# Performance work log

Hardware: AMD Instinct MI355X
Metric: run time of the kernel (lower is better)

## Reference

```python
import jax, jax.numpy as jnp
import numpy as np
from jax import lax

DIM = 192
HEADS = 4
EPS = 1e-12  # torch F.normalize eps


def setup_inputs() -> dict:
    key = jax.random.key(0)
    k1, k2, k3, k4 = jax.random.split(key, 4)
    b, c, h, w = 8, DIM, 128, 128
    x = jax.random.normal(k1, (b, c, h, w), dtype=jnp.float32)
    w_qkv = jax.random.normal(k2, (3 * c, c), dtype=jnp.float32) * (1.0 / np.sqrt(c))
    w_dw = jax.random.normal(k3, (3 * c, 1, 3, 3), dtype=jnp.float32) * (1.0 / 3.0)
    temperature = jnp.ones((HEADS, 1, 1), dtype=jnp.float32)
    w_proj = jax.random.normal(k4, (c, c), dtype=jnp.float32) * (1.0 / np.sqrt(c))
    return {"x": x, "w_qkv": w_qkv, "w_dw": w_dw, "temperature": temperature, "w_proj": w_proj}


def _l2norm(t):
    # torch F.normalize(dim=-1): t / max(||t||_2, eps)
    n = jnp.sqrt(jnp.sum(t * t, axis=-1, keepdims=True))
    return t / jnp.maximum(n, EPS)


def reference(x, w_qkv, w_dw, temperature, w_proj):
    b, c, h, w = x.shape
    heads = HEADS
    hc = c // heads  # channels per head
    # 1x1 conv: dim -> 3*dim
    qkv = jnp.einsum('bchw,oc->bohw', x, w_qkv)
    # depthwise 3x3 conv, padding=1, no relu/norm
    qkv = lax.conv_general_dilated(
        qkv, w_dw, window_strides=(1, 1), padding='SAME',
        feature_group_count=3 * c,
        dimension_numbers=('NCHW', 'OIHW', 'NCHW'))
    q, k, v = jnp.split(qkv, 3, axis=1)
    # b (head c) h w -> b head c (h w)
    n = h * w
    q = q.reshape(b, heads, hc, n)
    k = k.reshape(b, heads, hc, n)
    v = v.reshape(b, heads, hc, n)
    q = _l2norm(q)
    k = _l2norm(k)
    # channel attention: [b, head, hc, hc]
    attn = jnp.einsum('bhcn,bhdn->bhcd', q, k) * temperature[None]
    attn = jax.nn.softmax(attn, axis=-1)
    out = jnp.einsum('bhcd,bhdn->bhcn', attn, v)
    out = out.reshape(b, c, h, w)
    out = jnp.einsum('bchw,oc->bohw', out, w_proj)
    return out
```

## Files before the change

kernel.cpp:

```cpp
#include <hip/hip_runtime.h>
#include <stdint.h>


typedef __attribute__((ext_vector_type(8))) short bf16x8;
typedef __attribute__((ext_vector_type(4))) float f32x4;
typedef __attribute__((ext_vector_type(2))) float f32x2;
typedef __attribute__((ext_vector_type(4))) unsigned int u32x4;
typedef unsigned short u16;

#define HW 16384
#define CD 192
#define O3 576
#define KD 192

__device__ __forceinline__ float b2f(u16 u) {
    union { unsigned int i; float f; } v; v.i = ((unsigned int)u) << 16; return v.f;
}
__device__ __forceinline__ u16 f2b(float f) {
    union { float f; unsigned int i; } v; v.f = f;
    return (u16)((v.i + 0x7fffu + ((v.i >> 16) & 1u)) >> 16);
}

__global__ __launch_bounds__(256) void fill_f32(float* p, long long n, float val) {
    long long stride = (long long)gridDim.x * 256;
    for (long long i = blockIdx.x * 256LL + threadIdx.x; i < n; i += stride) p[i] = val;
}

__global__ __launch_bounds__(256) void zerof(float* p, int n) {
    int i = blockIdx.x * 256 + threadIdx.x;
    if (i < n) p[i] = 0.f;
}

__global__ __launch_bounds__(256) void afrag_prep(
    const float* __restrict__ W, u16* __restrict__ Af, int M, int NF)
{
    int t = blockIdx.x * 256 + threadIdx.x;
    if (t >= NF * 64) return;
    int F = t >> 6, lane = t & 63;
    int ks = F % 6, mt = (F / 6) & 3, rwmb = F / 24;
    int row = rwmb * 64 + mt * 16 + (lane & 15);
    int k0 = ks * 32 + (lane >> 4) * 8;
    u16 v[8] __attribute__((aligned(16)));
    if (row < M) {
        const float* src = W + (long long)row * KD + k0;
#pragma unroll
        for (int j = 0; j < 8; j++) v[j] = f2b(src[j]);
    } else {
#pragma unroll
        for (int j = 0; j < 8; j++) v[j] = 0;
    }
    *(bf16x8*)&Af[(long long)F * 512 + lane * 8] = *(const bf16x8*)v;
}

template <bool SRC_F32, bool OUT_F32>
__global__ __launch_bounds__(256, 2) void gemm_tn(
    const u16* __restrict__ Afrag, const void* __restrict__ Bsrc, void* __restrict__ Cv,
    int M, int nmb, long long af_bs, long long b_bs, long long c_bs)
{
    __shared__ u16 lsB[6][128 * 32];
    const int tid = threadIdx.x, lane = tid & 63, wid = tid >> 6;
    const int n0 = blockIdx.x * 128;
    const long long bz = blockIdx.z;
    const int lr = lane & 15, quad = lane >> 4;
    const int wm = (wid & 1) * 64, wn = (wid >> 1) * 64;

    {
        const int slot = wid ^ (lane & 3);
        u16* dA = &lsB[0][(2 * lane) * 32 + slot * 8];
        u16* dB = &lsB[0][(2 * lane + 1) * 32 + slot * 8];
        if (SRC_F32) {
            const float* gp = (const float*)Bsrc + bz * b_bs
                            + (long long)(wid * 8) * HW + n0 + 2 * lane;
#pragma unroll
            for (int ks = 0; ks < 6; ks++) {
                f32x2 rv[8];
#pragma unroll
                for (int j = 0; j < 8; j++) rv[j] = *(const f32x2*)(gp + (long long)j * HW);
                gp += 32LL * HW;
                unsigned int lo[4], hi[4];
#pragma unroll
                for (int i = 0; i < 4; i++) {
                    float a0 = rv[2 * i][0], b0 = rv[2 * i + 1][0];
                    float a1 = rv[2 * i][1], b1 = rv[2 * i + 1][1];
                    asm("v_cvt_pk_bf16_f32 %0, %1, %2" : "=v"(lo[i]) : "v"(a0), "v"(b0));
                    asm("v_cvt_pk_bf16_f32 %0, %1, %2" : "=v"(hi[i]) : "v"(a1), "v"(b1));
                }
                *(u32x4*)(dA + ks * 4096) = (u32x4){lo[0], lo[1], lo[2], lo[3]};
                *(u32x4*)(dB + ks * 4096) = (u32x4){hi[0], hi[1], hi[2], hi[3]};
            }
        } else {
            const u16* gp = (const u16*)Bsrc + bz * b_bs
                          + (long long)(wid * 8) * HW + n0 + 2 * lane;
#pragma unroll
            for (int ks = 0; ks < 6; ks++) {
                unsigned int rv[8];
#pragma unroll
                for (int j = 0; j < 8; j++) rv[j] = *(const unsigned int*)(gp + (long long)j * HW);
                gp += 32LL * HW;
                unsigned int lo[4], hi[4];
#pragma unroll
                for (int i = 0; i < 4; i++) {
                    lo[i] = (rv[2 * i] & 0xffffu) | (rv[2 * i + 1] << 16);
                    hi[i] = (rv[2 * i] >> 16) | (rv[2 * i + 1] & 0xffff0000u);
                }
                *(u32x4*)(dA + ks * 4096) = (u32x4){lo[0], lo[1], lo[2], lo[3]};
                *(u32x4*)(dB + ks * 4096) = (u32x4){hi[0], hi[1], hi[2], hi[3]};
            }
        }
    }
    __syncthreads();

    const int rslot = (quad ^ ((lr >> 1) & 3)) * 8;
    for (int mb = 0; mb < nmb; ++mb) {
        bf16x8 af[4][6];
        {
            const u16* Ap = Afrag + bz * af_bs
                          + ((long long)((mb * 2 + (wid & 1)) * 24)) * 512 + lane * 8;
#pragma unroll
            for (int mt = 0; mt < 4; mt++)
#pragma unroll
                for (int ks = 0; ks < 6; ks++)
                    af[mt][ks] = *(const bf16x8*)(Ap + (mt * 6 + ks) * 512);
        }
        f32x4 acc[4][4];
#pragma unroll
        for (int i = 0; i < 4; i++)
#pragma unroll
            for (int j = 0; j < 4; j++) acc[i][j] = (f32x4){0.f, 0.f, 0.f, 0.f};
#pragma unroll
        for (int ks = 0; ks < 6; ks++) {
            bf16x8 bfv[4];
#pragma unroll
            for (int nt = 0; nt < 4; nt++)
                bfv[nt] = *(const bf16x8*)&lsB[ks][(wn + nt * 16 + lr) * 32 + rslot];
#pragma unroll
            for (int mt = 0; mt < 4; mt++)
#pragma unroll
                for (int nt = 0; nt < 4; nt++)
                    acc[mt][nt] = __builtin_amdgcn_mfma_f32_16x16x32_bf16(af[mt][ks], bfv[nt], acc[mt][nt], 0, 0, 0);
        }
        const int m0 = mb * 128;
#pragma unroll
        for (int mt = 0; mt < 4; mt++)
#pragma unroll
            for (int r = 0; r < 4; r++) {
                int row = m0 + wm + mt * 16 + quad * 4 + r;
                if (row < M) {
#pragma unroll
                    for (int nt = 0; nt < 4; nt++) {
                        int col = n0 + wn + nt * 16 + lr;
                        if (OUT_F32)
                            ((float*)Cv)[bz * c_bs + (long long)row * HW + col] = acc[mt][nt][r];
                        else
                            ((u16*)Cv)[bz * c_bs + (long long)row * HW + col] = f2b(acc[mt][nt][r]);
                    }
                }
            }
    }
}

__global__ __launch_bounds__(256) void dwconv2(
    const u16* __restrict__ in, const float* __restrict__ wdw, u16* __restrict__ outp,
    long long in_bs, long long out_bs, int wch0)
{
    const int rt = blockIdx.x, ch = blockIdx.y, tid = threadIdx.x;
    const long long bz = blockIdx.z;
    const u16* ip = in + bz * in_bs + (long long)ch * HW;
    u16* op = outp + bz * out_bs + (long long)ch * HW;
    __shared__ float t[18 * 132];
    const int r0 = rt * 16;
    if (tid < 18) {
        t[tid * 132 + 0] = 0.f;   t[tid * 132 + 129] = 0.f;
        t[tid * 132 + 130] = 0.f; t[tid * 132 + 131] = 0.f;
    }
    for (int i = tid; i < 288; i += 256) {
        int rr = i >> 4, cc = (i & 15) * 8;
        int gr = r0 + rr - 1;
        float f[8];
        if (gr >= 0 && gr < 128) {
            bf16x8 v = *(const bf16x8*)(ip + gr * 128 + cc);
#pragma unroll
            for (int j = 0; j < 8; j++) f[j] = b2f((u16)v[j]);
        } else {
#pragma unroll
            for (int j = 0; j < 8; j++) f[j] = 0.f;
        }
#pragma unroll
        for (int j = 0; j < 8; j++) t[rr * 132 + 1 + cc + j] = f[j];
    }
    float w[9];
#pragma unroll
    for (int j = 0; j < 9; j++) w[j] = wdw[(wch0 + ch) * 9 + j];
    __syncthreads();
    const int rr = tid >> 4, c8 = (tid & 15) * 8;
    float o[8] = {0.f, 0.f, 0.f, 0.f, 0.f, 0.f, 0.f, 0.f};
#pragma unroll
    for (int dy = 0; dy < 3; dy++) {
        const float* row = &t[(rr + dy) * 132 + c8];
        float r[12] __attribute__((aligned(16)));
        *(f32x4*)&r[0] = *(const f32x4*)row;
        *(f32x4*)&r[4] = *(const f32x4*)(row + 4);
        *(f32x4*)&r[8] = *(const f32x4*)(row + 8);
        const float w0 = w[dy * 3], w1 = w[dy * 3 + 1], w2 = w[dy * 3 + 2];
#pragma unroll
        for (int j = 0; j < 8; j++) o[j] += w0 * r[j] + w1 * r[j + 1] + w2 * r[j + 2];
    }
    u16 ob[8] __attribute__((aligned(16)));
#pragma unroll
    for (int j = 0; j < 8; j++) ob[j] = f2b(o[j]);
    *(bf16x8*)&op[(long long)(r0 + rr) * 128 + c8] = *(const bf16x8*)ob;
}

__global__ __launch_bounds__(256) void attn_scores(
    const u16* __restrict__ qk, float* __restrict__ S, float* __restrict__ norms,
    int bh0)
{
    const int tid = threadIdx.x, lane = tid & 63, wid = tid >> 6;
    const int kc = blockIdx.x, head = blockIdx.y;
    const long long bz = blockIdx.z;
    const u16* q = qk + bz * (2LL * CD * HW) + (long long)head * 48 * HW;
    const u16* k = q + (long long)CD * HW;
    const int lr = lane & 15, quad = lane >> 4;

    f32x4 sc[3][3], sq[3], sk[3];
#pragma unroll
    for (int i = 0; i < 3; i++) {
#pragma unroll
        for (int j = 0; j < 3; j++) sc[i][j] = (f32x4){0.f, 0.f, 0.f, 0.f};
        sq[i] = (f32x4){0.f, 0.f, 0.f, 0.f};
        sk[i] = (f32x4){0.f, 0.f, 0.f, 0.f};
    }
    const int n0 = kc * 1024 + wid * 256;
#pragma unroll 2
    for (int s = 0; s < 8; s++) {
        const int n = n0 + s * 32 + quad * 8;
        bf16x8 aq[3], ak[3];
#pragma unroll
        for (int t3 = 0; t3 < 3; t3++) {
            aq[t3] = *(const bf16x8*)(q + (long long)(t3 * 16 + lr) * HW + n);
            ak[t3] = *(const bf16x8*)(k + (long long)(t3 * 16 + lr) * HW + n);
        }
#pragma unroll
        for (int mt = 0; mt < 3; mt++)
#pragma unroll
            for (int nt = 0; nt < 3; nt++)
                sc[mt][nt] = __builtin_amdgcn_mfma_f32_16x16x32_bf16(aq[mt], ak[nt], sc[mt][nt], 0, 0, 0);
#pragma unroll
        for (int t3 = 0; t3 < 3; t3++) {
            sq[t3] = __builtin_amdgcn_mfma_f32_16x16x32_bf16(aq[t3], aq[t3], sq[t3], 0, 0, 0);
            sk[t3] = __builtin_amdgcn_mfma_f32_16x16x32_bf16(ak[t3], ak[t3], sk[t3], 0, 0, 0);
        }
    }
    __shared__ float sS[2304];
    __shared__ float snq[48], snk[48];
    for (int i = tid; i < 2304; i += 256) sS[i] = 0.f;
    if (tid < 48) { snq[tid] = 0.f; snk[tid] = 0.f; }
    __syncthreads();
#pragma unroll
    for (int mt = 0; mt < 3; mt++)
#pragma unroll
        for (int nt = 0; nt < 3; nt++)
#pragma unroll
            for (int r = 0; r < 4; r++)
                atomicAdd(&sS[(mt * 16 + quad * 4 + r) * 48 + nt * 16 + lr], sc[mt][nt][r]);
#pragma unroll
    for (int t3 = 0; t3 < 3; t3++)
#pragma unroll
        for (int r = 0; r < 4; r++) {
            int rw = quad * 4 + r;
            if (rw == lr) {
                atomicAdd(&snq[t3 * 16 + rw], sq[t3][r]);
                atomicAdd(&snk[t3 * 16 + rw], sk[t3][r]);
            }
        }
    __syncthreads();
    const int bh = bh0 + (int)bz * 4 + head;
    float* Sg = S + (long long)bh * 2304;
    for (int i = tid; i < 2304; i += 256) atomicAdd(&Sg[i], sS[i]);
    float* ng = norms + bh * 96;
    if (tid < 48) atomicAdd(&ng[tid], snq[tid]);
    else if (tid < 96) atomicAdd(&ng[tid], snk[tid - 48]);
}

__global__ __launch_bounds__(64) void softmax_k(
    const float* __restrict__ S, const float* __restrict__ norms,
    const float* __restrict__ temp, float* __restrict__ attn, int bh0)
{
    const int bh = bh0 + blockIdx.x, head = bh & 3, r = threadIdx.x;
    if (r >= 48) return;
    const float tv = temp[head];
    const float* Sg = S + (long long)bh * 2304;
    const float* ng = norms + bh * 96;
    const float nq = fmaxf(sqrtf(ng[r]), 1e-12f);
    float lg[48];
    float mx = -1e30f;
#pragma unroll
    for (int d = 0; d < 48; d++) {
        float nk = fmaxf(sqrtf(ng[48 + d]), 1e-12f);
        float v = Sg[r * 48 + d] * tv / (nq * nk);
        lg[d] = v; mx = fmaxf(mx, v);
    }
    float sum = 0.f;
#pragma unroll
    for (int d = 0; d < 48; d++) { float e = __expf(lg[d] - mx); lg[d] = e; sum += e; }
    const float inv = 1.f / sum;
    float* Ag = attn + (long long)bh * 2304 + r * 48;
#pragma unroll
    for (int d = 0; d < 48; d++) Ag[d] = lg[d] * inv;
}

__global__ __launch_bounds__(256) void mproj(
    const float* __restrict__ wproj, const float* __restrict__ attn, u16* __restrict__ Mm,
    int b0)
{
    const int ob = blockIdx.x, b = b0 + blockIdx.y, tid = threadIdx.x;
    __shared__ float sA[9216];
    const float* Ab = attn + (long long)b * 9216;
    for (int i = tid; i < 9216; i += 256) sA[i] = Ab[i];
    __syncthreads();
    for (int i = tid; i < 48 * 192; i += 256) {
        int o = ob * 48 + i / 192;
        int cc = i % 192;
        int h = cc / 48, d = cc - h * 48;
        const float* wr = wproj + o * 192 + h * 48;
        const float* ar = &sA[h * 2304 + d];
        float acc = 0.f;
        for (int c = 0; c < 48; c++) acc += wr[c] * ar[c * 48];
        int fi = (o >> 6) * 24 + ((o >> 4) & 3) * 6 + (cc >> 5);
        int lanei = ((cc >> 3) & 3) * 16 + (o & 15);
        Mm[(long long)b * 49152 + (long long)fi * 512 + lanei * 8 + (cc & 7)] = f2b(acc);
    }
}

extern "C" void kernel_launch(void* const* d_in, const int* in_sizes, int n_in,
                              void* d_out, int out_size, void* d_ws, size_t ws_size,
                              hipStream_t stream)
{
    const float* x     = (const float*)d_in[0];
    const float* wqkv  = (const float*)d_in[1];
    const float* wdw   = (const float*)d_in[2];
    const float* temp  = (const float*)d_in[3];
    const float* wproj = (const float*)d_in[4];
    float* out = (float*)d_out;
    char* ws = (char*)d_ws;
    const long long CHW = (long long)CD * HW;

    if (ws_size < 2097152ULL + 31457280ULL) {
        fill_f32<<<2048, 256, 0, stream>>>(out, out_size, 100.0f);
        return;
    }
    int G = 8;
    while (G > 1 && (unsigned long long)(2097152ULL + (unsigned long long)G * 31457280ULL) > (unsigned long long)ws_size)
        G >>= 1;

    float* S      = (float*)ws;
    float* norms  = (float*)(ws + 294912);
    float* attn   = (float*)(ws + 307200);
    u16*   MmF    = (u16*)(ws + 602112);
    u16*   wqkvF  = (u16*)(ws + 1388544);
    u16* region1  = (u16*)(ws + 2097152);
    u16* qkv_pre  = region1 + (long long)G * 2 * CHW;

    zerof<<<300, 256, 0, stream>>>(S, 76800);
    afrag_prep<<<60, 256, 0, stream>>>(wqkv, wqkvF, O3, 240);

    for (int g0 = 0; g0 < 8; g0 += G) {
        gemm_tn<true, false><<<dim3(128, 1, G), 256, 0, stream>>>(
            wqkvF, x + (long long)g0 * CHW, qkv_pre, O3, 5, 0LL, CHW, 3LL * CHW);
        dwconv2<<<dim3(8, 384, G), 256, 0, stream>>>(
            qkv_pre, wdw, region1, 3LL * CHW, 2LL * CHW, 0);
        dwconv2<<<dim3(8, 192, G), 256, 0, stream>>>(
            qkv_pre + 2LL * CHW, wdw, qkv_pre, 3LL * CHW, 3LL * CHW, 384);
        attn_scores<<<dim3(16, 4, G), 256, 0, stream>>>(region1, S, norms, g0 * 4);
        softmax_k<<<4 * G, 64, 0, stream>>>(S, norms, temp, attn, g0 * 4);
        mproj<<<dim3(4, G), 256, 0, stream>>>(wproj, attn, MmF, g0);
        gemm_tn<false, true><<<dim3(128, 1, G), 256, 0, stream>>>(
            MmF + (long long)g0 * 49152, qkv_pre, out + (long long)g0 * CHW,
            CD, 2, 49152LL, 3LL * CHW, CHW);
    }
}
```

Before: 410.2 us.

## Halve GEMM N-tile to 64 columns and double grid, compile-time M-block count

```diff
diff --git a/kernel.cpp b/kernel.cpp
--- a/kernel.cpp
+++ b/kernel.cpp
@@ -52,79 +52,88 @@
     *(bf16x8*)&Af[(long long)F * 512 + lane * 8] = *(const bf16x8*)v;
 }
 
-template <bool SRC_F32, bool OUT_F32>
+template <bool SRC_F32, bool OUT_F32, int NMB>
 __global__ __launch_bounds__(256, 2) void gemm_tn(
     const u16* __restrict__ Afrag, const void* __restrict__ Bsrc, void* __restrict__ Cv,
-    int M, int nmb, long long af_bs, long long b_bs, long long c_bs)
-{
-    __shared__ u16 lsB[6][128 * 32];
+    int M, long long af_bs, long long b_bs, long long c_bs)
+{
+    __shared__ u16 lsB[6][64 * 32];
     const int tid = threadIdx.x, lane = tid & 63, wid = tid >> 6;
-    const int n0 = blockIdx.x * 128;
+    const int n0 = blockIdx.x * 64;
     const long long bz = blockIdx.z;
     const int lr = lane & 15, quad = lane >> 4;
-    const int wm = (wid & 1) * 64, wn = (wid >> 1) * 64;
 
     {
-        const int slot = wid ^ (lane & 3);
-        u16* dA = &lsB[0][(2 * lane) * 32 + slot * 8];
-        u16* dB = &lsB[0][(2 * lane + 1) * 32 + slot * 8];
+        const int kg = tid >> 5, l5 = tid & 31;
+        const int slot = (kg & 3) ^ (l5 & 3);
+        u16* dA = &lsB[0][(2 * l5) * 32 + slot * 8];
         if (SRC_F32) {
             const float* gp = (const float*)Bsrc + bz * b_bs
-                            + (long long)(wid * 8) * HW + n0 + 2 * lane;
-#pragma unroll
-            for (int ks = 0; ks < 6; ks++) {
-                f32x2 rv[8];
-#pragma unroll
-                for (int j = 0; j < 8; j++) rv[j] = *(const f32x2*)(gp + (long long)j * HW);
-                gp += 32LL * HW;
+                            + (long long)(kg * 8) * HW + n0 + 2 * l5;
+            f32x2 rv[24];
+#pragma unroll
+            for (int r = 0; r < 3; r++)
+#pragma unroll
+                for (int j = 0; j < 8; j++)
+                    rv[r * 8 + j] = *(const f32x2*)(gp + ((long long)r * 64 + j) * HW);
+#pragma unroll
+            for (int r = 0; r < 3; r++) {
                 unsigned int lo[4], hi[4];
 #pragma unroll
                 for (int i = 0; i < 4; i++) {
-                    float a0 = rv[2 * i][0], b0 = rv[2 * i + 1][0];
-                    float a1 = rv[2 * i][1], b1 = rv[2 * i + 1][1];
+                    float a0 = rv[r * 8 + 2 * i][0], b0 = rv[r * 8 + 2 * i + 1][0];
+                    float a1 = rv[r * 8 + 2 * i][1], b1 = rv[r * 8 + 2 * i + 1][1];
                     asm("v_cvt_pk_bf16_f32 %0, %1, %2" : "=v"(lo[i]) : "v"(a0), "v"(b0));
                     asm("v_cvt_pk_bf16_f32 %0, %1, %2" : "=v"(hi[i]) : "v"(a1), "v"(b1));
                 }
-                *(u32x4*)(dA + ks * 4096) = (u32x4){lo[0], lo[1], lo[2], lo[3]};
-                *(u32x4*)(dB + ks * 4096) = (u32x4){hi[0], hi[1], hi[2], hi[3]};
+                const int ck = r * 2 + (kg >> 2);
+                *(u32x4*)(dA + ck * 2048)      = (u32x4){lo[0], lo[1], lo[2], lo[3]};
+                *(u32x4*)(dA + ck * 2048 + 32) = (u32x4){hi[0], hi[1], hi[2], hi[3]};
             }
         } else {
             const u16* gp = (const u16*)Bsrc + bz * b_bs
-                          + (long long)(wid * 8) * HW + n0 + 2 * lane;
-#pragma unroll
-            for (int ks = 0; ks < 6; ks++) {
-                unsigned int rv[8];
-#pragma unroll
-                for (int j = 0; j < 8; j++) rv[j] = *(const unsigned int*)(gp + (long long)j * HW);
-                gp += 32LL * HW;
+                          + (long long)(kg * 8) * HW + n0 + 2 * l5;
+            unsigned int rv[24];
+#pragma unroll
+            for (int r = 0; r < 3; r++)
+#pragma unroll
+                for (int j = 0; j < 8; j++)
+                    rv[r * 8 + j] = *(const unsigned int*)(gp + ((long long)r * 64 + j) * HW);
+#pragma unroll
+            for (int r = 0; r < 3; r++) {
                 unsigned int lo[4], hi[4];
 #pragma unroll
                 for (int i = 0; i < 4; i++) {
-                    lo[i] = (rv[2 * i] & 0xffffu) | (rv[2 * i + 1] << 16);
-                    hi[i] = (rv[2 * i] >> 16) | (rv[2 * i + 1] & 0xffff0000u);
+                    unsigned int e = rv[r * 8 + 2 * i], o = rv[r * 8 + 2 * i + 1];
+                    lo[i] = (e & 0xffffu) | (o << 16);
+                    hi[i] = (e >> 16) | (o & 0xffff0000u);
                 }
-                *(u32x4*)(dA + ks * 4096) = (u32x4){lo[0], lo[1], lo[2], lo[3]};
-                *(u32x4*)(dB + ks * 4096) = (u32x4){hi[0], hi[1], hi[2], hi[3]};
+                const int ck = r * 2 + (kg >> 2);
+                *(u32x4*)(dA + ck * 2048)      = (u32x4){lo[0], lo[1], lo[2], lo[3]};
+                *(u32x4*)(dA + ck * 2048 + 32) = (u32x4){hi[0], hi[1], hi[2], hi[3]};
             }
         }
     }
     __syncthreads();
 
     const int rslot = (quad ^ ((lr >> 1) & 3)) * 8;
-    for (int mb = 0; mb < nmb; ++mb) {
-        bf16x8 af[4][6];
+#pragma unroll
+    for (int mb = 0; mb < NMB; ++mb) {
+        const int wmBase = mb * 128 + wid * 32;
+        if (wmBase >= M) continue;
+        bf16x8 af[2][6];
         {
             const u16* Ap = Afrag + bz * af_bs
-                          + ((long long)((mb * 2 + (wid & 1)) * 24)) * 512 + lane * 8;
-#pragma unroll
-            for (int mt = 0; mt < 4; mt++)
+                          + ((long long)((mb * 2 + (wid >> 1)) * 24)) * 512 + lane * 8;
+#pragma unroll
+            for (int mtl = 0; mtl < 2; mtl++)
 #pragma unroll
                 for (int ks = 0; ks < 6; ks++)
-                    af[mt][ks] = *(const bf16x8*)(Ap + (mt * 6 + ks) * 512);
-        }
-        f32x4 acc[4][4];
-#pragma unroll
-        for (int i = 0; i < 4; i++)
+                    af[mtl][ks] = *(const bf16x8*)(Ap + (((wid & 1) * 2 + mtl) * 6 + ks) * 512);
+        }
+        f32x4 acc[2][4];
+#pragma unroll
+        for (int i = 0; i < 2; i++)
 #pragma unroll
             for (int j = 0; j < 4; j++) acc[i][j] = (f32x4){0.f, 0.f, 0.f, 0.f};
 #pragma unroll
@@ -132,27 +141,26 @@
             bf16x8 bfv[4];
 #pragma unroll
             for (int nt = 0; nt < 4; nt++)
-                bfv[nt] = *(const bf16x8*)&lsB[ks][(wn + nt * 16 + lr) * 32 + rslot];
-#pragma unroll
-            for (int mt = 0; mt < 4; mt++)
+                bfv[nt] = *(const bf16x8*)&lsB[ks][(nt * 16 + lr) * 32 + rslot];
+#pragma unroll
+            for (int mtl = 0; mtl < 2; mtl++)
 #pragma unroll
                 for (int nt = 0; nt < 4; nt++)
-                    acc[mt][nt] = __builtin_amdgcn_mfma_f32_16x16x32_bf16(af[mt][ks], bfv[nt], acc[mt][nt], 0, 0, 0);
-        }
-        const int m0 = mb * 128;
-#pragma unroll
-        for (int mt = 0; mt < 4; mt++)
+                    acc[mtl][nt] = __builtin_amdgcn_mfma_f32_16x16x32_bf16(af[mtl][ks], bfv[nt], acc[mtl][nt], 0, 0, 0);
+        }
+#pragma unroll
+        for (int mtl = 0; mtl < 2; mtl++)
 #pragma unroll
             for (int r = 0; r < 4; r++) {
-                int row = m0 + wm + mt * 16 + quad * 4 + r;
+                int row = wmBase + mtl * 16 + quad * 4 + r;
                 if (row < M) {
 #pragma unroll
                     for (int nt = 0; nt < 4; nt++) {
-                        int col = n0 + wn + nt * 16 + lr;
+                        int col = n0 + nt * 16 + lr;
                         if (OUT_F32)
-                            ((float*)Cv)[bz * c_bs + (long long)row * HW + col] = acc[mt][nt][r];
+                            ((float*)Cv)[bz * c_bs + (long long)row * HW + col] = acc[mtl][nt][r];
                         else
-                            ((u16*)Cv)[bz * c_bs + (long long)row * HW + col] = f2b(acc[mt][nt][r]);
+                            ((u16*)Cv)[bz * c_bs + (long long)row * HW + col] = f2b(acc[mtl][nt][r]);
                     }
                 }
             }
@@ -365,8 +373,8 @@
     afrag_prep<<<60, 256, 0, stream>>>(wqkv, wqkvF, O3, 240);
 
     for (int g0 = 0; g0 < 8; g0 += G) {
-        gemm_tn<true, false><<<dim3(128, 1, G), 256, 0, stream>>>(
-            wqkvF, x + (long long)g0 * CHW, qkv_pre, O3, 5, 0LL, CHW, 3LL * CHW);
+        gemm_tn<true, false, 5><<<dim3(256, 1, G), 256, 0, stream>>>(
+            wqkvF, x + (long long)g0 * CHW, qkv_pre, O3, 0LL, CHW, 3LL * CHW);
         dwconv2<<<dim3(8, 384, G), 256, 0, stream>>>(
             qkv_pre, wdw, region1, 3LL * CHW, 2LL * CHW, 0);
         dwconv2<<<dim3(8, 192, G), 256, 0, stream>>>(
@@ -374,8 +382,8 @@
         attn_scores<<<dim3(16, 4, G), 256, 0, stream>>>(region1, S, norms, g0 * 4);
         softmax_k<<<4 * G, 64, 0, stream>>>(S, norms, temp, attn, g0 * 4);
         mproj<<<dim3(4, G), 256, 0, stream>>>(wproj, attn, MmF, g0);
-        gemm_tn<false, true><<<dim3(128, 1, G), 256, 0, stream>>>(
+        gemm_tn<false, true, 2><<<dim3(256, 1, G), 256, 0, stream>>>(
             MmF + (long long)g0 * 49152, qkv_pre, out + (long long)g0 * CHW,
-            CD, 2, 49152LL, 3LL * CHW, CHW);
-    }
-}
+            CD, 49152LL, 3LL * CHW, CHW);
+    }
+}
```

Measured after the change: 408.1 us. No clear change (-0.5%).

## Restructure GEMM: register-resident B fragments, wide staged loads, double-buffered A

Applied to the files above, without the earlier changes.

```diff
diff --git a/kernel.cpp b/kernel.cpp
--- a/kernel.cpp
+++ b/kernel.cpp
@@ -6,6 +6,7 @@
 typedef __attribute__((ext_vector_type(4))) float f32x4;
 typedef __attribute__((ext_vector_type(2))) float f32x2;
 typedef __attribute__((ext_vector_type(4))) unsigned int u32x4;
+typedef __attribute__((ext_vector_type(2))) unsigned int u32x2;
 typedef unsigned short u16;
 
 #define HW 16384
@@ -52,111 +53,140 @@
     *(bf16x8*)&Af[(long long)F * 512 + lane * 8] = *(const bf16x8*)v;
 }
 
-template <bool SRC_F32, bool OUT_F32>
+template <bool SRC_F32, bool OUT_F32, int NMS>
 __global__ __launch_bounds__(256, 2) void gemm_tn(
     const u16* __restrict__ Afrag, const void* __restrict__ Bsrc, void* __restrict__ Cv,
-    int M, int nmb, long long af_bs, long long b_bs, long long c_bs)
-{
-    __shared__ u16 lsB[6][128 * 32];
+    long long af_bs, long long b_bs, long long c_bs)
+{
+    __shared__ u16 lsB[128 * 192];
     const int tid = threadIdx.x, lane = tid & 63, wid = tid >> 6;
     const int n0 = blockIdx.x * 128;
     const long long bz = blockIdx.z;
     const int lr = lane & 15, quad = lane >> 4;
-    const int wm = (wid & 1) * 64, wn = (wid >> 1) * 64;
-
-    {
-        const int slot = wid ^ (lane & 3);
-        u16* dA = &lsB[0][(2 * lane) * 32 + slot * 8];
-        u16* dB = &lsB[0][(2 * lane + 1) * 32 + slot * 8];
-        if (SRC_F32) {
-            const float* gp = (const float*)Bsrc + bz * b_bs
-                            + (long long)(wid * 8) * HW + n0 + 2 * lane;
-#pragma unroll
-            for (int ks = 0; ks < 6; ks++) {
-                f32x2 rv[8];
-#pragma unroll
-                for (int j = 0; j < 8; j++) rv[j] = *(const f32x2*)(gp + (long long)j * HW);
-                gp += 32LL * HW;
-                unsigned int lo[4], hi[4];
-#pragma unroll
-                for (int i = 0; i < 4; i++) {
-                    float a0 = rv[2 * i][0], b0 = rv[2 * i + 1][0];
-                    float a1 = rv[2 * i][1], b1 = rv[2 * i + 1][1];
-                    asm("v_cvt_pk_bf16_f32 %0, %1, %2" : "=v"(lo[i]) : "v"(a0), "v"(b0));
-                    asm("v_cvt_pk_bf16_f32 %0, %1, %2" : "=v"(hi[i]) : "v"(a1), "v"(b1));
-                }
-                *(u32x4*)(dA + ks * 4096) = (u32x4){lo[0], lo[1], lo[2], lo[3]};
-                *(u32x4*)(dB + ks * 4096) = (u32x4){hi[0], hi[1], hi[2], hi[3]};
-            }
-        } else {
-            const u16* gp = (const u16*)Bsrc + bz * b_bs
-                          + (long long)(wid * 8) * HW + n0 + 2 * lane;
-#pragma unroll
-            for (int ks = 0; ks < 6; ks++) {
-                unsigned int rv[8];
-#pragma unroll
-                for (int j = 0; j < 8; j++) rv[j] = *(const unsigned int*)(gp + (long long)j * HW);
-                gp += 32LL * HW;
-                unsigned int lo[4], hi[4];
-#pragma unroll
-                for (int i = 0; i < 4; i++) {
-                    lo[i] = (rv[2 * i] & 0xffffu) | (rv[2 * i + 1] << 16);
-                    hi[i] = (rv[2 * i] >> 16) | (rv[2 * i + 1] & 0xffff0000u);
-                }
-                *(u32x4*)(dA + ks * 4096) = (u32x4){lo[0], lo[1], lo[2], lo[3]};
-                *(u32x4*)(dB + ks * 4096) = (u32x4){hi[0], hi[1], hi[2], hi[3]};
-            }
-        }
+    const int wn = wid & 1, wm = wid >> 1;
+
+#define LADDR(n_, ks_) ((n_) * 192 + (((ks_) ^ (((n_) >> 2) & 7)) * 8))
+
+    if (SRC_F32) {
+        const int c32 = lane & 31, rs = lane >> 5;
+        const float* gp = (const float*)Bsrc + bz * b_bs + n0 + 4 * c32;
+        f32x4 bufA[8], bufB[8];
+#define LOADC_F(buf, c) do { \
+    const float* p_ = gp + (long long)((c) * 64 + wid * 16 + rs * 8) * HW; \
+    _Pragma("unroll") for (int i_ = 0; i_ < 8; i_++) \
+        buf[i_] = *(const f32x4*)(p_ + (long long)i_ * HW); \
+} while (0)
+#define PROC_F(buf, c) do { \
+    const int kslot_ = (c) * 8 + wid * 2 + rs; \
+    _Pragma("unroll") for (int j_ = 0; j_ < 4; j_++) { \
+        const int n_ = 4 * c32 + j_; \
+        unsigned int p0_, p1_, p2_, p3_; \
+        asm("v_cvt_pk_bf16_f32 %0, %1, %2" : "=v"(p0_) : "v"(buf[0][j_]), "v"(buf[1][j_])); \
+        asm("v_cvt_pk_bf16_f32 %0, %1, %2" : "=v"(p1_) : "v"(buf[2][j_]), "v"(buf[3][j_])); \
+        asm("v_cvt_pk_bf16_f32 %0, %1, %2" : "=v"(p2_) : "v"(buf[4][j_]), "v"(buf[5][j_])); \
+        asm("v_cvt_pk_bf16_f32 %0, %1, %2" : "=v"(p3_) : "v"(buf[6][j_]), "v"(buf[7][j_])); \
+        *(u32x4*)&lsB[LADDR(n_, kslot_)] = (u32x4){p0_, p1_, p2_, p3_}; \
+    } \
+} while (0)
+        LOADC_F(bufA, 0);
+        LOADC_F(bufB, 1);
+        __builtin_amdgcn_sched_barrier(0);
+        PROC_F(bufA, 0);
+        LOADC_F(bufA, 2);
+        __builtin_amdgcn_sched_barrier(0);
+        PROC_F(bufB, 1);
+        PROC_F(bufA, 2);
+#undef LOADC_F
+#undef PROC_F
+    } else {
+        const int c16 = lane & 15, rs4 = lane >> 4;
+        const u16* gp = (const u16*)Bsrc + bz * b_bs + n0 + 8 * c16;
+        u32x4 bufA[4], bufB[4];
+#define LOADC_B(buf, c) do { \
+    const u16* p_ = gp + (long long)((c) * 64 + wid * 16 + rs4 * 4) * HW; \
+    _Pragma("unroll") for (int i_ = 0; i_ < 4; i_++) \
+        buf[i_] = *(const u32x4*)(p_ + (long long)i_ * HW); \
+} while (0)
+#define PROC_B(buf, c) do { \
+    const int kslot_ = (c) * 8 + wid * 2 + (rs4 >> 1); \
+    const int kh_ = (rs4 & 1) * 4; \
+    _Pragma("unroll") for (int j_ = 0; j_ < 4; j_++) { \
+        unsigned int l0_ = __builtin_amdgcn_perm(buf[0][j_], buf[1][j_], 0x01000504u); \
+        unsigned int l1_ = __builtin_amdgcn_perm(buf[2][j_], buf[3][j_], 0x01000504u); \
+        unsigned int h0_ = __builtin_amdgcn_perm(buf[0][j_], buf[1][j_], 0x03020706u); \
+        unsigned int h1_ = __builtin_amdgcn_perm(buf[2][j_], buf[3][j_], 0x03020706u); \
+        *(u32x2*)&lsB[LADDR(8 * c16 + 2 * j_, kslot_) + kh_] = (u32x2){l0_, l1_}; \
+        *(u32x2*)&lsB[LADDR(8 * c16 + 2 * j_ + 1, kslot_) + kh_] = (u32x2){h0_, h1_}; \
+    } \
+} while (0)
+        LOADC_B(bufA, 0);
+        LOADC_B(bufB, 1);
+        __builtin_amdgcn_sched_barrier(0);
+        PROC_B(bufA, 0);
+        LOADC_B(bufA, 2);
+        __builtin_amdgcn_sched_barrier(0);
+        PROC_B(bufB, 1);
+        PROC_B(bufA, 2);
+#undef LOADC_B
+#undef PROC_B
     }
     __syncthreads();
 
-    const int rslot = (quad ^ ((lr >> 1) & 3)) * 8;
-    for (int mb = 0; mb < nmb; ++mb) {
-        bf16x8 af[4][6];
-        {
-            const u16* Ap = Afrag + bz * af_bs
-                          + ((long long)((mb * 2 + (wid & 1)) * 24)) * 512 + lane * 8;
-#pragma unroll
-            for (int mt = 0; mt < 4; mt++)
-#pragma unroll
-                for (int ks = 0; ks < 6; ks++)
-                    af[mt][ks] = *(const bf16x8*)(Ap + (mt * 6 + ks) * 512);
-        }
-        f32x4 acc[4][4];
-#pragma unroll
-        for (int i = 0; i < 4; i++)
-#pragma unroll
-            for (int j = 0; j < 4; j++) acc[i][j] = (f32x4){0.f, 0.f, 0.f, 0.f};
-#pragma unroll
-        for (int ks = 0; ks < 6; ks++) {
-            bf16x8 bfv[4];
-#pragma unroll
-            for (int nt = 0; nt < 4; nt++)
-                bfv[nt] = *(const bf16x8*)&lsB[ks][(wn + nt * 16 + lr) * 32 + rslot];
-#pragma unroll
-            for (int mt = 0; mt < 4; mt++)
-#pragma unroll
-                for (int nt = 0; nt < 4; nt++)
-                    acc[mt][nt] = __builtin_amdgcn_mfma_f32_16x16x32_bf16(af[mt][ks], bfv[nt], acc[mt][nt], 0, 0, 0);
-        }
-        const int m0 = mb * 128;
-#pragma unroll
-        for (int mt = 0; mt < 4; mt++)
-#pragma unroll
-            for (int r = 0; r < 4; r++) {
-                int row = m0 + wm + mt * 16 + quad * 4 + r;
-                if (row < M) {
-#pragma unroll
-                    for (int nt = 0; nt < 4; nt++) {
-                        int col = n0 + wn + nt * 16 + lr;
-                        if (OUT_F32)
-                            ((float*)Cv)[bz * c_bs + (long long)row * HW + col] = acc[mt][nt][r];
-                        else
-                            ((u16*)Cv)[bz * c_bs + (long long)row * HW + col] = f2b(acc[mt][nt][r]);
-                    }
-                }
-            }
-    }
+    bf16x8 bfv[6][4];
+#pragma unroll
+    for (int ks = 0; ks < 6; ks++)
+#pragma unroll
+        for (int nt = 0; nt < 4; nt++) {
+            const int n_ = wn * 64 + nt * 16 + lr;
+            bfv[ks][nt] = *(const bf16x8*)&lsB[LADDR(n_, ks * 4 + quad)];
+        }
+#undef LADDR
+
+    const u16* ApBase = Afrag + bz * af_bs + lane * 8;
+    const long long cB = bz * c_bs + n0 + wn * 64 + lr;
+    constexpr int NT = NMS / 2;
+
+#define LOAD_AF(dst, sv) do { \
+    _Pragma("unroll") for (int mtl_ = 0; mtl_ < 2; mtl_++) \
+    _Pragma("unroll") for (int ks_ = 0; ks_ < 6; ks_++) \
+        dst[mtl_][ks_] = *(const bf16x8*)(ApBase + \
+            (long long)(((sv) >> 1) * 24 + (((sv) & 1) * 2 + mtl_) * 6 + ks_) * 512); \
+} while (0)
+#define COMPUTE_MB(afb, sv) do { \
+    f32x4 acc_[2][4]; \
+    _Pragma("unroll") for (int i_ = 0; i_ < 2; i_++) \
+    _Pragma("unroll") for (int j_ = 0; j_ < 4; j_++) \
+        acc_[i_][j_] = (f32x4){0.f, 0.f, 0.f, 0.f}; \
+    _Pragma("unroll") for (int ks_ = 0; ks_ < 6; ks_++) \
+    _Pragma("unroll") for (int mtl_ = 0; mtl_ < 2; mtl_++) \
+    _Pragma("unroll") for (int nt_ = 0; nt_ < 4; nt_++) \
+        acc_[mtl_][nt_] = __builtin_amdgcn_mfma_f32_16x16x32_bf16( \
+            afb[mtl_][ks_], bfv[ks_][nt_], acc_[mtl_][nt_], 0, 0, 0); \
+    _Pragma("unroll") for (int mtl_ = 0; mtl_ < 2; mtl_++) \
+    _Pragma("unroll") for (int r_ = 0; r_ < 4; r_++) { \
+        const long long ro_ = cB + (long long)(32 * (sv) + mtl_ * 16 + quad * 4 + r_) * HW; \
+        _Pragma("unroll") for (int nt_ = 0; nt_ < 4; nt_++) { \
+            if (OUT_F32) ((float*)Cv)[ro_ + nt_ * 16] = acc_[mtl_][nt_][r_]; \
+            else         ((u16*)Cv)[ro_ + nt_ * 16] = f2b(acc_[mtl_][nt_][r_]); \
+        } \
+    } \
+} while (0)
+
+    bf16x8 afA[2][6], afB[2][6];
+    const int s0 = wm * NT;
+    LOAD_AF(afA, s0);
+#pragma unroll
+    for (int t = 0; t < NT; ++t) {
+        if (t + 1 < NT) {
+            if (t & 1) LOAD_AF(afA, s0 + t + 1);
+            else       LOAD_AF(afB, s0 + t + 1);
+            __builtin_amdgcn_sched_barrier(0);
+        }
+        if (t & 1) COMPUTE_MB(afB, s0 + t);
+        else       COMPUTE_MB(afA, s0 + t);
+    }
+#undef LOAD_AF
+#undef COMPUTE_MB
 }
 
 __global__ __launch_bounds__(256) void dwconv2(
@@ -365,8 +395,8 @@
     afrag_prep<<<60, 256, 0, stream>>>(wqkv, wqkvF, O3, 240);
 
     for (int g0 = 0; g0 < 8; g0 += G) {
-        gemm_tn<true, false><<<dim3(128, 1, G), 256, 0, stream>>>(
-            wqkvF, x + (long long)g0 * CHW, qkv_pre, O3, 5, 0LL, CHW, 3LL * CHW);
+        gemm_tn<true, false, 18><<<dim3(128, 1, G), 256, 0, stream>>>(
+            wqkvF, x + (long long)g0 * CHW, qkv_pre, 0LL, CHW, 3LL * CHW);
         dwconv2<<<dim3(8, 384, G), 256, 0, stream>>>(
             qkv_pre, wdw, region1, 3LL * CHW, 2LL * CHW, 0);
         dwconv2<<<dim3(8, 192, G), 256, 0, stream>>>(
@@ -374,8 +404,8 @@
         attn_scores<<<dim3(16, 4, G), 256, 0, stream>>>(region1, S, norms, g0 * 4);
         softmax_k<<<4 * G, 64, 0, stream>>>(S, norms, temp, attn, g0 * 4);
         mproj<<<dim3(4, G), 256, 0, stream>>>(wproj, attn, MmF, g0);
-        gemm_tn<false, true><<<dim3(128, 1, G), 256, 0, stream>>>(
+        gemm_tn<false, true, 6><<<dim3(128, 1, G), 256, 0, stream>>>(
             MmF + (long long)g0 * 49152, qkv_pre, out + (long long)g0 * CHW,
-            CD, 2, 49152LL, 3LL * CHW, CHW);
-    }
-}
+            49152LL, 3LL * CHW, CHW);
+    }
+}
```

Result: faster. 390.2 us (-4.9%).
